# Kernel optimization log

Measured on AMD Instinct MI355X. Metric: run time of the kernel, lower is better.

The kernel has to match this reference:

```python
import jax, jax.numpy as jnp
import numpy as np

B, S, E, A = 8, 127, 512, 256  # batch, seq (pre-sentinel), encoder dim, arc representation dim

_BRANCHES = ["sib_head", "sib_dep", "cop_head", "cop_dep", "gp_head", "gp_dep", "gp_head_dep"]


def setup_inputs() -> dict:
    key = jax.random.key(0)
    ks = jax.random.split(key, 16)
    d = {
        "x": jax.random.normal(ks[0], (B, S, E), jnp.float32),
        "pos_tags": jax.random.randint(ks[1], (B, S), 0, 48),
        "mask": jnp.ones((B, S), jnp.int32),
    }
    for i, n in enumerate(_BRANCHES):
        d[f"W_{n}"] = jax.random.normal(ks[2 + i], (E, A), jnp.float32) * (1.0 / np.sqrt(E))
        d[f"b_{n}"] = jnp.zeros((A,), jnp.float32)
    for i, n in enumerate(["sib", "cop", "gp"]):
        d[f"U_{n}"] = jax.random.normal(ks[9 + i], (A, A, A), jnp.float32) * (1.0 / A)
    d["sentinel"] = jax.random.normal(ks[12], (E,), jnp.float32)
    return d


def _tri(u, v, w, U):
    # trilinear (triaffine) score: s[b,i,j,k] = sum_{a,c,d} u[b,i,a] U[a,c,d] v[b,j,c] w[b,k,d]
    t = jnp.einsum('bia,acd->bicd', u, U)       # [B, n, A, A]
    t = jnp.einsum('bicd,bjc->bijd', t, v)      # [B, n, n, A]
    return jnp.einsum('bijd,bkd->bijk', t, w)   # [B, n, n, n]


def reference(x, pos_tags, mask,
              W_sib_head, b_sib_head, W_sib_dep, b_sib_dep,
              W_cop_head, b_cop_head, W_cop_dep, b_cop_dep,
              W_gp_head, b_gp_head, W_gp_dep, b_gp_dep,
              W_gp_head_dep, b_gp_head_dep,
              U_sib, U_cop, U_gp, sentinel):
    b, _, e = x.shape
    # prepend head sentinel token
    h = jnp.concatenate([jnp.broadcast_to(sentinel, (b, 1, e)), x], axis=1)  # [B, n, E]
    mask_full = jnp.concatenate([jnp.ones((b, 1), mask.dtype), mask], axis=1)
    elu = jax.nn.elu
    sib_head = elu(h @ W_sib_head + b_sib_head)
    sib_dep = elu(h @ W_sib_dep + b_sib_dep)
    cop_head = elu(h @ W_cop_head + b_cop_head)
    cop_dep = elu(h @ W_cop_dep + b_cop_dep)
    gp_head = elu(h @ W_gp_head + b_gp_head)
    gp_dep = elu(h @ W_gp_dep + b_gp_dep)
    gp_head_dep = elu(h @ W_gp_head_dep + b_gp_head_dep)
    sib = _tri(sib_head, sib_dep, sib_dep, U_sib)
    cop = _tri(cop_head, cop_dep, cop_head, U_cop)
    gp = _tri(gp_head, gp_head_dep, gp_dep, U_gp)
    return sib, cop, gp, mask_full
```

## Files before the change

kernel.cpp:

```cpp
#include <hip/hip_runtime.h>
#include <math.h>

#define N_TOK 128
#define ADIM  256
#define EDIM  512
#define BSZ   8
#define NSQ   65536
#define PAD   40

typedef short bf16x8 __attribute__((ext_vector_type(8)));
typedef float f32x4  __attribute__((ext_vector_type(4)));
#define MFMA_BF16(a, b, c) __builtin_amdgcn_mfma_f32_16x16x32_bf16((a), (b), (c), 0, 0, 0)

__device__ inline short f2bf(float f) {
  union { float f; unsigned u; } v; v.f = f;
  unsigned r = v.u + 0x7fff + ((v.u >> 16) & 1);
  return (short)(r >> 16);
}

struct ProjArgs {
  const float* W[7];
  const float* b[7];
};

__global__ __launch_bounds__(256) void proj_kernel(
    const float* __restrict__ x, const float* __restrict__ sentinel,
    ProjArgs args, short* __restrict__ proj)
{
  const int p  = blockIdx.y;
  const int m0 = blockIdx.x * 8;
  const int tid = threadIdx.x;
  __shared__ float hs[8][EDIM];
  #pragma unroll
  for (int q = 0; q < 16; ++q) {
    int idx = tid + q * 256;
    int r = idx >> 9, c = idx & 511;
    int m = m0 + r, b = m >> 7, i = m & 127;
    hs[r][c] = (i == 0) ? sentinel[c] : x[((size_t)(b * 127) + (i - 1)) * EDIM + c];
  }
  __syncthreads();
  const float* W = args.W[p];
  float bias = args.b[p][tid];
  float acc[8];
  #pragma unroll
  for (int r = 0; r < 8; ++r) acc[r] = bias;
  #pragma unroll 4
  for (int k = 0; k < EDIM; ++k) {
    float wv = W[(size_t)k * ADIM + tid];
    #pragma unroll
    for (int r = 0; r < 8; ++r) acc[r] = fmaf(hs[r][k], wv, acc[r]);
  }
  short* outp = proj + ((size_t)p * (BSZ * N_TOK) + m0) * ADIM + tid;
  #pragma unroll
  for (int r = 0; r < 8; ++r) {
    float v = acc[r];
    v = v > 0.f ? v : expm1f(v);
    outp[(size_t)r * ADIM] = f2bf(v);
  }
}

__global__ __launch_bounds__(256) void permU(
    const float* __restrict__ U, short* __restrict__ Ut)
{
  __shared__ float tile[64][69];
  const int c  = blockIdx.x;
  const int a0 = blockIdx.y * 64;
  const int d0 = blockIdx.z * 64;
  const int t  = threadIdx.x;
  {
    int ar = t >> 4, ds4 = (t & 15) * 4;
    #pragma unroll
    for (int q = 0; q < 4; ++q) {
      int a = ar + q * 16;
      float4 v = *(const float4*)&U[(size_t)(a0 + a) * NSQ + c * 256 + d0 + ds4];
      tile[a][ds4] = v.x; tile[a][ds4 + 1] = v.y;
      tile[a][ds4 + 2] = v.z; tile[a][ds4 + 3] = v.w;
    }
  }
  __syncthreads();
  {
    int dr = t >> 4, as4 = (t & 15) * 4;
    #pragma unroll
    for (int q = 0; q < 4; ++q) {
      int d = dr + q * 16;
      ushort4 o;
      o.x = (unsigned short)f2bf(tile[as4 + 0][d]);
      o.y = (unsigned short)f2bf(tile[as4 + 1][d]);
      o.z = (unsigned short)f2bf(tile[as4 + 2][d]);
      o.w = (unsigned short)f2bf(tile[as4 + 3][d]);
      *(ushort4*)&Ut[((size_t)(d0 + d) * 256 + c) * 256 + a0 + as4] = o;
    }
  }
}

__global__ __launch_bounds__(256) void gemm_t1(
    const short* __restrict__ A,
    const short* __restrict__ Ut,
    short* __restrict__ C)
{
  __shared__ short As[128][PAD];
  __shared__ short Bs[128][PAD];
  const int tid = threadIdx.x;
  const int wave = tid >> 6, lane = tid & 63;
  const int ln15 = lane & 15, quad = lane >> 4;
  const int m0 = blockIdx.x * 128, n0 = blockIdx.y * 128;
  const int wm = (wave & 1) * 64, wn = (wave >> 1) * 64;
  f32x4 acc[4][4] = {};
  for (int kt = 0; kt < ADIM; kt += 32) {
    __syncthreads();
    #pragma unroll
    for (int p = 0; p < 2; ++p) {
      int q = tid + p * 256;
      int r = q >> 2, s = q & 3;
      *(uint4*)&As[r][s * 8] = *(const uint4*)&A [(size_t)(m0 + r) * ADIM + kt + s * 8];
      *(uint4*)&Bs[r][s * 8] = *(const uint4*)&Ut[(size_t)(n0 + r) * ADIM + kt + s * 8];
    }
    __syncthreads();
    bf16x8 af[4], bfr[4];
    #pragma unroll
    for (int r = 0; r < 4; ++r)  af[r]  = *(bf16x8*)&As[wm + r * 16 + ln15][quad * 8];
    #pragma unroll
    for (int c2 = 0; c2 < 4; ++c2) bfr[c2] = *(bf16x8*)&Bs[wn + c2 * 16 + ln15][quad * 8];
    #pragma unroll
    for (int r = 0; r < 4; ++r)
      #pragma unroll
      for (int c2 = 0; c2 < 4; ++c2)
        acc[r][c2] = MFMA_BF16(af[r], bfr[c2], acc[r][c2]);
  }
  #pragma unroll
  for (int r = 0; r < 4; ++r)
    #pragma unroll
    for (int c2 = 0; c2 < 4; ++c2)
      #pragma unroll
      for (int e = 0; e < 4; ++e) {
        int m = m0 + wm + r * 16 + quad * 4 + e;
        int n = n0 + wn + c2 * 16 + ln15;
        C[(size_t)m * NSQ + n] = f2bf(acc[r][c2][e]);
      }
}

__global__ __launch_bounds__(256) void gemm_t2(
    const short* __restrict__ t1,
    const short* __restrict__ projv,
    short* __restrict__ t2,
    int b0)
{
  __shared__ short As[128][PAD];
  __shared__ short Bs[128][PAD];
  const int tid = threadIdx.x;
  const int wave = tid >> 6, lane = tid & 63;
  const int ln15 = lane & 15, quad = lane >> 4;
  const int n0 = blockIdx.x * 128;
  const int bl = blockIdx.y;
  const int b  = b0 + bl;
  const short* Bt = t1 + (size_t)bl * N_TOK * NSQ;
  const short* Av = projv + (size_t)b * N_TOK * ADIM;
  const int wm = (wave & 1) * 64, wn = (wave >> 1) * 64;
  f32x4 acc[4][4] = {};
  for (int kt = 0; kt < ADIM; kt += 32) {
    __syncthreads();
    #pragma unroll
    for (int p = 0; p < 2; ++p) {
      int q = tid + p * 256;
      int r = q >> 2, s = q & 3;
      *(uint4*)&As[r][s * 8] = *(const uint4*)&Av[(size_t)r * ADIM + kt + s * 8];
      *(uint4*)&Bs[r][s * 8] = *(const uint4*)&Bt[(size_t)(n0 + r) * ADIM + kt + s * 8];
    }
    __syncthreads();
    bf16x8 af[4], bfr[4];
    #pragma unroll
    for (int r = 0; r < 4; ++r)  af[r]  = *(bf16x8*)&As[wm + r * 16 + ln15][quad * 8];
    #pragma unroll
    for (int c2 = 0; c2 < 4; ++c2) bfr[c2] = *(bf16x8*)&Bs[wn + c2 * 16 + ln15][quad * 8];
    #pragma unroll
    for (int r = 0; r < 4; ++r)
      #pragma unroll
      for (int c2 = 0; c2 < 4; ++c2)
        acc[r][c2] = MFMA_BF16(af[r], bfr[c2], acc[r][c2]);
  }
  const int i     = n0 >> 8;
  const int dbase = n0 & 255;
  short* ob = t2 + (size_t)bl * (N_TOK * N_TOK * ADIM) + (size_t)i * (N_TOK * ADIM);
  #pragma unroll
  for (int r = 0; r < 4; ++r)
    #pragma unroll
    for (int c2 = 0; c2 < 4; ++c2)
      #pragma unroll
      for (int e = 0; e < 4; ++e) {
        int j = wm + r * 16 + quad * 4 + e;
        int d = dbase + wn + c2 * 16 + ln15;
        ob[(size_t)j * ADIM + d] = f2bf(acc[r][c2][e]);
      }
}

__global__ __launch_bounds__(256) void gemm_s(
    const short* __restrict__ t2,
    const short* __restrict__ projw,
    float* __restrict__ out,
    int b0)
{
  __shared__ short As[128][PAD];
  __shared__ short Bs[128][PAD];
  const int tid = threadIdx.x;
  const int wave = tid >> 6, lane = tid & 63;
  const int ln15 = lane & 15, quad = lane >> 4;
  const int m0 = blockIdx.x * 128;
  const int bl = blockIdx.y;
  const int b  = b0 + bl;
  const short* At = t2 + (size_t)bl * (N_TOK * N_TOK * ADIM);
  const short* Bw = projw + (size_t)b * N_TOK * ADIM;
  float* ob = out + (size_t)b * N_TOK * N_TOK * N_TOK + (size_t)m0 * N_TOK;
  const int wm = (wave & 1) * 64, wn = (wave >> 1) * 64;
  f32x4 acc[4][4] = {};
  for (int kt = 0; kt < ADIM; kt += 32) {
    __syncthreads();
    #pragma unroll
    for (int p = 0; p < 2; ++p) {
      int q = tid + p * 256;
      int r = q >> 2, s = q & 3;
      *(uint4*)&As[r][s * 8] = *(const uint4*)&At[(size_t)(m0 + r) * ADIM + kt + s * 8];
      *(uint4*)&Bs[r][s * 8] = *(const uint4*)&Bw[(size_t)r * ADIM + kt + s * 8];
    }
    __syncthreads();
    bf16x8 af[4], bfr[4];
    #pragma unroll
    for (int r = 0; r < 4; ++r)  af[r]  = *(bf16x8*)&As[wm + r * 16 + ln15][quad * 8];
    #pragma unroll
    for (int c2 = 0; c2 < 4; ++c2) bfr[c2] = *(bf16x8*)&Bs[wn + c2 * 16 + ln15][quad * 8];
    #pragma unroll
    for (int r = 0; r < 4; ++r)
      #pragma unroll
      for (int c2 = 0; c2 < 4; ++c2)
        acc[r][c2] = MFMA_BF16(af[r], bfr[c2], acc[r][c2]);
  }
  #pragma unroll
  for (int r = 0; r < 4; ++r)
    #pragma unroll
    for (int c2 = 0; c2 < 4; ++c2)
      #pragma unroll
      for (int e = 0; e < 4; ++e) {
        int m = wm + r * 16 + quad * 4 + e;
        int k = wn + c2 * 16 + ln15;
        ob[(size_t)m * N_TOK + k] = acc[r][c2][e];
      }
}

__global__ void mask_kernel(const int* __restrict__ mask, float* __restrict__ out) {
  int idx = blockIdx.x * 256 + threadIdx.x;
  if (idx < BSZ * N_TOK) {
    int b = idx >> 7, i = idx & 127;
    out[idx] = (i == 0) ? 1.0f : (float)mask[b * 127 + i - 1];
  }
}

extern "C" void kernel_launch(void* const* d_in, const int* in_sizes, int n_in,
                              void* d_out, int out_size, void* d_ws, size_t ws_size,
                              hipStream_t stream)
{
  const float* x    = (const float*)d_in[0];
  const int*   mask = (const int*)d_in[2];
  ProjArgs pa;
  for (int p = 0; p < 7; ++p) {
    pa.W[p] = (const float*)d_in[3 + 2 * p];
    pa.b[p] = (const float*)d_in[4 + 2 * p];
  }
  const float* Us[3] = {(const float*)d_in[17], (const float*)d_in[18],
                        (const float*)d_in[19]};
  const float* sentinel = (const float*)d_in[20];

  short* proj = (short*)d_ws;
  const size_t ut_off = 4u << 20;
  const size_t t1_off = ut_off + ((size_t)NSQ * ADIM * 2);
  short* Ut = (short*)((char*)d_ws + ut_off);
  size_t avail = (ws_size > t1_off) ? ws_size - t1_off : 0;
  const size_t t1_chunk = (size_t)N_TOK * NSQ * 2;
  const size_t t2_chunk = (size_t)N_TOK * N_TOK * ADIM * 2;
  int cb = 8;
  while (cb > 1 && (size_t)cb * (t1_chunk + t2_chunk) > avail) cb >>= 1;
  short* t1 = (short*)((char*)d_ws + t1_off);
  short* t2 = (short*)((char*)d_ws + t1_off + (size_t)cb * t1_chunk);

  proj_kernel<<<dim3(128, 7), 256, 0, stream>>>(x, sentinel, pa, proj);

  const int u_idx[3] = {0, 2, 4};
  const int v_idx[3] = {1, 3, 6};
  const int w_idx[3] = {1, 2, 5};
  float* outp = (float*)d_out;

  for (int sc = 0; sc < 3; ++sc) {
    permU<<<dim3(256, 4, 4), 256, 0, stream>>>(Us[sc], Ut);
    for (int b0 = 0; b0 < BSZ; b0 += cb) {
      const short* A = proj + ((size_t)u_idx[sc] * 1024 + (size_t)b0 * N_TOK) * ADIM;
      gemm_t1<<<dim3(cb, 512), 256, 0, stream>>>(A, Ut, t1);
      gemm_t2<<<dim3(256, cb), 256, 0, stream>>>(
          t1, proj + (size_t)v_idx[sc] * 1024 * ADIM, t2, b0);
      gemm_s<<<dim3(128, cb), 256, 0, stream>>>(
          t2, proj + (size_t)w_idx[sc] * 1024 * ADIM,
          outp + (size_t)sc * BSZ * N_TOK * N_TOK * N_TOK, b0);
    }
  }
  mask_kernel<<<dim3(4), 256, 0, stream>>>(
      mask, outp + (size_t)3 * BSZ * N_TOK * N_TOK * N_TOK);
}
```

Before: 898.3 us.

## Chunk the d dimension to process full batch per launch, vectorize GEMM stores

Splits the trilinear U tensor along the d axis into chunks so the t1 intermediate for all 8 batches fits in workspace, replacing the batch-chunk loop with a d-chunk loop and a single final contraction per score. Swaps the MFMA operand order so each lane holds four contiguous output columns, which allows 8-byte bf16 and 16-byte fp32 vector stores instead of scalar strided stores. The goal is larger grids, fewer small launches, and more efficient global writes. In exchange, permU and the t1/t2 GEMMs run twice per score, and workspace sizing is now fixed rather than adapted to ws_size.

```diff
diff --git a/kernel.cpp b/kernel.cpp
--- a/kernel.cpp
+++ b/kernel.cpp
@@ -6,6 +6,8 @@
 #define EDIM  512
 #define BSZ   8
 #define NSQ   65536
+#define DCH   128
+#define NCH   (DCH * 256)
 #define PAD   40
 
 typedef short bf16x8 __attribute__((ext_vector_type(8)));
@@ -60,7 +62,7 @@
 }
 
 __global__ __launch_bounds__(256) void permU(
-    const float* __restrict__ U, short* __restrict__ Ut)
+    const float* __restrict__ U, short* __restrict__ Ut, int d0c)
 {
   __shared__ float tile[64][69];
   const int c  = blockIdx.x;
@@ -72,7 +74,7 @@
     #pragma unroll
     for (int q = 0; q < 4; ++q) {
       int a = ar + q * 16;
-      float4 v = *(const float4*)&U[(size_t)(a0 + a) * NSQ + c * 256 + d0 + ds4];
+      float4 v = *(const float4*)&U[(size_t)(a0 + a) * NSQ + c * 256 + d0c + d0 + ds4];
       tile[a][ds4] = v.x; tile[a][ds4 + 1] = v.y;
       tile[a][ds4 + 2] = v.z; tile[a][ds4 + 3] = v.w;
     }
@@ -125,25 +127,28 @@
     for (int r = 0; r < 4; ++r)
       #pragma unroll
       for (int c2 = 0; c2 < 4; ++c2)
-        acc[r][c2] = MFMA_BF16(af[r], bfr[c2], acc[r][c2]);
+        acc[r][c2] = MFMA_BF16(bfr[c2], af[r], acc[r][c2]);
   }
   #pragma unroll
   for (int r = 0; r < 4; ++r)
     #pragma unroll
-    for (int c2 = 0; c2 < 4; ++c2)
-      #pragma unroll
-      for (int e = 0; e < 4; ++e) {
-        int m = m0 + wm + r * 16 + quad * 4 + e;
-        int n = n0 + wn + c2 * 16 + ln15;
-        C[(size_t)m * NSQ + n] = f2bf(acc[r][c2][e]);
-      }
+    for (int c2 = 0; c2 < 4; ++c2) {
+      int m = m0 + wm + r * 16 + ln15;
+      int n = n0 + wn + c2 * 16 + quad * 4;
+      ushort4 o;
+      o.x = (unsigned short)f2bf(acc[r][c2][0]);
+      o.y = (unsigned short)f2bf(acc[r][c2][1]);
+      o.z = (unsigned short)f2bf(acc[r][c2][2]);
+      o.w = (unsigned short)f2bf(acc[r][c2][3]);
+      *(ushort4*)&C[(size_t)m * NCH + n] = o;
+    }
 }
 
 __global__ __launch_bounds__(256) void gemm_t2(
-    const short* __restrict__ t1,
+    const short* __restrict__ t1c,
     const short* __restrict__ projv,
     short* __restrict__ t2,
-    int b0)
+    int d0c)
 {
   __shared__ short As[128][PAD];
   __shared__ short Bs[128][PAD];
@@ -152,9 +157,8 @@
   const int ln15 = lane & 15, quad = lane >> 4;
   const int n0 = blockIdx.x * 128;
   const int bl = blockIdx.y;
-  const int b  = b0 + bl;
-  const short* Bt = t1 + (size_t)bl * N_TOK * NSQ;
-  const short* Av = projv + (size_t)b * N_TOK * ADIM;
+  const short* Bt = t1c + (size_t)bl * N_TOK * NCH;
+  const short* Av = projv + (size_t)bl * N_TOK * ADIM;
   const int wm = (wave & 1) * 64, wn = (wave >> 1) * 64;
   f32x4 acc[4][4] = {};
   for (int kt = 0; kt < ADIM; kt += 32) {
@@ -176,28 +180,29 @@
     for (int r = 0; r < 4; ++r)
       #pragma unroll
       for (int c2 = 0; c2 < 4; ++c2)
-        acc[r][c2] = MFMA_BF16(af[r], bfr[c2], acc[r][c2]);
-  }
-  const int i     = n0 >> 8;
-  const int dbase = n0 & 255;
-  short* ob = t2 + (size_t)bl * (N_TOK * N_TOK * ADIM) + (size_t)i * (N_TOK * ADIM);
+        acc[r][c2] = MFMA_BF16(bfr[c2], af[r], acc[r][c2]);
+  }
+  const int i = n0 >> 7;
+  short* ob = t2 + (size_t)bl * (N_TOK * N_TOK * ADIM) + (size_t)i * (N_TOK * ADIM) + d0c;
   #pragma unroll
   for (int r = 0; r < 4; ++r)
     #pragma unroll
-    for (int c2 = 0; c2 < 4; ++c2)
-      #pragma unroll
-      for (int e = 0; e < 4; ++e) {
-        int j = wm + r * 16 + quad * 4 + e;
-        int d = dbase + wn + c2 * 16 + ln15;
-        ob[(size_t)j * ADIM + d] = f2bf(acc[r][c2][e]);
-      }
+    for (int c2 = 0; c2 < 4; ++c2) {
+      int j  = wm + r * 16 + ln15;
+      int dl = wn + c2 * 16 + quad * 4;
+      ushort4 o;
+      o.x = (unsigned short)f2bf(acc[r][c2][0]);
+      o.y = (unsigned short)f2bf(acc[r][c2][1]);
+      o.z = (unsigned short)f2bf(acc[r][c2][2]);
+      o.w = (unsigned short)f2bf(acc[r][c2][3]);
+      *(ushort4*)&ob[(size_t)j * ADIM + dl] = o;
+    }
 }
 
 __global__ __launch_bounds__(256) void gemm_s(
     const short* __restrict__ t2,
     const short* __restrict__ projw,
-    float* __restrict__ out,
-    int b0)
+    float* __restrict__ out)
 {
   __shared__ short As[128][PAD];
   __shared__ short Bs[128][PAD];
@@ -206,10 +211,9 @@
   const int ln15 = lane & 15, quad = lane >> 4;
   const int m0 = blockIdx.x * 128;
   const int bl = blockIdx.y;
-  const int b  = b0 + bl;
   const short* At = t2 + (size_t)bl * (N_TOK * N_TOK * ADIM);
-  const short* Bw = projw + (size_t)b * N_TOK * ADIM;
-  float* ob = out + (size_t)b * N_TOK * N_TOK * N_TOK + (size_t)m0 * N_TOK;
+  const short* Bw = projw + (size_t)bl * N_TOK * ADIM;
+  float* ob = out + (size_t)bl * N_TOK * N_TOK * N_TOK + (size_t)m0 * N_TOK;
   const int wm = (wave & 1) * 64, wn = (wave >> 1) * 64;
   f32x4 acc[4][4] = {};
   for (int kt = 0; kt < ADIM; kt += 32) {
@@ -231,18 +235,16 @@
     for (int r = 0; r < 4; ++r)
       #pragma unroll
       for (int c2 = 0; c2 < 4; ++c2)
-        acc[r][c2] = MFMA_BF16(af[r], bfr[c2], acc[r][c2]);
+        acc[r][c2] = MFMA_BF16(bfr[c2], af[r], acc[r][c2]);
   }
   #pragma unroll
   for (int r = 0; r < 4; ++r)
     #pragma unroll
-    for (int c2 = 0; c2 < 4; ++c2)
-      #pragma unroll
-      for (int e = 0; e < 4; ++e) {
-        int m = wm + r * 16 + quad * 4 + e;
-        int k = wn + c2 * 16 + ln15;
-        ob[(size_t)m * N_TOK + k] = acc[r][c2][e];
-      }
+    for (int c2 = 0; c2 < 4; ++c2) {
+      int m = wm + r * 16 + ln15;
+      int k = wn + c2 * 16 + quad * 4;
+      *(f32x4*)&ob[(size_t)m * N_TOK + k] = acc[r][c2];
+    }
 }
 
 __global__ void mask_kernel(const int* __restrict__ mask, float* __restrict__ out) {
@@ -270,15 +272,11 @@
 
   short* proj = (short*)d_ws;
   const size_t ut_off = 4u << 20;
-  const size_t t1_off = ut_off + ((size_t)NSQ * ADIM * 2);
-  short* Ut = (short*)((char*)d_ws + ut_off);
-  size_t avail = (ws_size > t1_off) ? ws_size - t1_off : 0;
-  const size_t t1_chunk = (size_t)N_TOK * NSQ * 2;
-  const size_t t2_chunk = (size_t)N_TOK * N_TOK * ADIM * 2;
-  int cb = 8;
-  while (cb > 1 && (size_t)cb * (t1_chunk + t2_chunk) > avail) cb >>= 1;
-  short* t1 = (short*)((char*)d_ws + t1_off);
-  short* t2 = (short*)((char*)d_ws + t1_off + (size_t)cb * t1_chunk);
+  const size_t t1_off = ut_off + ((size_t)NCH * 256 * 2);
+  const size_t t2_off = t1_off + ((size_t)1024 * NCH * 2);
+  short* Utc = (short*)((char*)d_ws + ut_off);
+  short* t1c = (short*)((char*)d_ws + t1_off);
+  short* t2  = (short*)((char*)d_ws + t2_off);
 
   proj_kernel<<<dim3(128, 7), 256, 0, stream>>>(x, sentinel, pa, proj);
 
@@ -288,16 +286,17 @@
   float* outp = (float*)d_out;
 
   for (int sc = 0; sc < 3; ++sc) {
-    permU<<<dim3(256, 4, 4), 256, 0, stream>>>(Us[sc], Ut);
-    for (int b0 = 0; b0 < BSZ; b0 += cb) {
-      const short* A = proj + ((size_t)u_idx[sc] * 1024 + (size_t)b0 * N_TOK) * ADIM;
-      gemm_t1<<<dim3(cb, 512), 256, 0, stream>>>(A, Ut, t1);
-      gemm_t2<<<dim3(256, cb), 256, 0, stream>>>(
-          t1, proj + (size_t)v_idx[sc] * 1024 * ADIM, t2, b0);
-      gemm_s<<<dim3(128, cb), 256, 0, stream>>>(
-          t2, proj + (size_t)w_idx[sc] * 1024 * ADIM,
-          outp + (size_t)sc * BSZ * N_TOK * N_TOK * N_TOK, b0);
-    }
+    for (int ch = 0; ch < 256 / DCH; ++ch) {
+      const int d0c = ch * DCH;
+      permU<<<dim3(256, 4, DCH / 64), 256, 0, stream>>>(Us[sc], Utc, d0c);
+      gemm_t1<<<dim3(8, NCH / 128), 256, 0, stream>>>(
+          proj + (size_t)u_idx[sc] * 1024 * ADIM, Utc, t1c);
+      gemm_t2<<<dim3(128, 8), 256, 0, stream>>>(
+          t1c, proj + (size_t)v_idx[sc] * 1024 * ADIM, t2, d0c);
+    }
+    gemm_s<<<dim3(128, 8), 256, 0, stream>>>(
+        t2, proj + (size_t)w_idx[sc] * 1024 * ADIM,
+        outp + (size_t)sc * BSZ * N_TOK * N_TOK * N_TOK);
   }
   mask_kernel<<<dim3(4), 256, 0, stream>>>(
       mask, outp + (size_t)3 * BSZ * N_TOK * N_TOK * N_TOK);
```

After: 969.4 us. +7.9%, slower.
